# Optimization experiments

Hardware: AMD Instinct MI355X
Metric: run time of the kernel (lower is better)

## Reference

```python
import jax, jax.numpy as jnp
import numpy as np

B, S, F = 64, 1024, 768          # batch, seq = num_patch*patch_size**2, d_model
H, DH = 12, 64                    # heads, head dim = out_dim // d
P2 = 64                           # patch_size ** 2 = attended window length
SCALE = 8.0                       # norm_scale ** 0.5 = (out_dim // d) ** 0.5


def setup_inputs() -> dict:
    key = jax.random.key(0)
    ks = jax.random.split(key, 10)
    std = 0.02
    return {
        "x": jax.random.normal(ks[0], (B, S, F), dtype=jnp.float32),
        # per-head q/k/v projection weights stacked: [H, DH, F] (Linear: y = x @ W.T + b)
        "Wq": jax.random.normal(ks[1], (H, DH, F), dtype=jnp.float32) * std,
        "bq": jax.random.normal(ks[2], (H, DH), dtype=jnp.float32) * std,
        "Wk": jax.random.normal(ks[3], (H, DH, F), dtype=jnp.float32) * std,
        "bk": jax.random.normal(ks[4], (H, DH), dtype=jnp.float32) * std,
        "Wv": jax.random.normal(ks[5], (H, DH, F), dtype=jnp.float32) * std,
        "bv": jax.random.normal(ks[6], (H, DH), dtype=jnp.float32) * std,
        # MHA output projection (only W_MSA[0] is ever used in the stage1 path)
        "Wo": jax.random.normal(ks[7], (F, F), dtype=jnp.float32) * std,
        "bo": jax.random.normal(ks[8], (F,), dtype=jnp.float32) * std,
    }


def reference(x, Wq, bq, Wk, bk, Wv, bv, Wo, bo):
    # stage1 path of SBlock1: only the first window (P2 tokens) goes through
    # MultiHeadAttention (W_MSA[0]); remaining windows are passed through raw
    # and concatenated along the sequence dim.
    xw = x[:, :P2, :]                                    # [B, P2, F]
    q = jnp.einsum('bsf,hdf->bhsd', xw, Wq) + bq[None, :, None, :]
    k = jnp.einsum('bsf,hdf->bhsd', xw, Wk) + bk[None, :, None, :]
    v = jnp.einsum('bsf,hdf->bhsd', xw, Wv) + bv[None, :, None, :]
    scores = jnp.einsum('bhsd,bhtd->bhst', q, k) / SCALE
    attn = jax.nn.softmax(scores, axis=-1)
    o = jnp.einsum('bhst,bhtd->bhsd', attn, v)           # [B, H, P2, DH]
    # heads concatenated along feature dim in order 0..H-1
    o = o.transpose(0, 2, 1, 3).reshape(xw.shape[0], P2, H * DH)
    o = o @ Wo.T + bo                                    # output projection
    return jnp.concatenate([o, x[:, P2:, :]], axis=1)    # [B, S, F]
```

## Files before the change

kernel.cpp:

```cpp
#include <hip/hip_runtime.h>

#define B_   64
#define S_   1024
#define F_   768
#define H_   12
#define DH_  64
#define P2_  64
#define NQKV 2304

using bf16x8 = __attribute__((ext_vector_type(8))) short;
using f32x4  = __attribute__((ext_vector_type(4))) float;

__device__ __forceinline__ unsigned short f2bf(float f) {
    union { float f; unsigned u; } v;
    v.f = f;
    unsigned r = v.u + 0x7FFF + ((v.u >> 16) & 1);
    return (unsigned short)(r >> 16);
}

__device__ __forceinline__ void gll16(const unsigned short* g, unsigned char* l) {
    __builtin_amdgcn_global_load_lds(
        (const __attribute__((address_space(1))) unsigned int*)g,
        (__attribute__((address_space(3))) unsigned int*)l, 16, 0, 0);
}

__device__ __forceinline__ void copy_role(const float* __restrict__ x,
                                          float* __restrict__ out,
                                          int off4, int cnt4, int nblk, int bid) {
    int stride = nblk * 256;
    for (int i = bid * 256 + threadIdx.x; i < cnt4; i += stride) {
        int j = off4 + i;
        int b = j / 184320, r = j - b * 184320;
        int idx = b * 196608 + 12288 + r;
        reinterpret_cast<float4*>(out)[idx] =
            reinterpret_cast<const float4*>(x)[idx];
    }
}

__global__ __launch_bounds__(256) void prep_kernel(
        const float* __restrict__ x,
        const float* __restrict__ Wq, const float* __restrict__ Wk,
        const float* __restrict__ Wv, const float* __restrict__ Wo,
        const float* __restrict__ bq, const float* __restrict__ bk,
        const float* __restrict__ bv,
        unsigned short* __restrict__ xw, unsigned short* __restrict__ Wqkv,
        unsigned short* __restrict__ Wob, float* __restrict__ bqv) {
    const int NW = 786432;
    const int W4 = 147456;
    int i = blockIdx.x * 256 + threadIdx.x;
    if (i < NW) {
        int b = i / 12288, r = i - b * 12288;
        float4 v = reinterpret_cast<const float4*>(x)[b * 196608 + r];
        ushort4 h;
        h.x = f2bf(v.x); h.y = f2bf(v.y); h.z = f2bf(v.z); h.w = f2bf(v.w);
        reinterpret_cast<ushort4*>(xw)[i] = h;
    } else if (i < NW + 3 * W4) {
        int j = i - NW;
        int which = j / W4, local = j - which * W4;
        const float* src = (which == 0) ? Wq : (which == 1) ? Wk : Wv;
        float4 v = reinterpret_cast<const float4*>(src)[local];
        ushort4 h;
        h.x = f2bf(v.x); h.y = f2bf(v.y); h.z = f2bf(v.z); h.w = f2bf(v.w);
        reinterpret_cast<ushort4*>(Wqkv)[j] = h;
    } else if (i < NW + 4 * W4) {
        int local = i - NW - 3 * W4;
        float4 v = reinterpret_cast<const float4*>(Wo)[local];
        ushort4 h;
        h.x = f2bf(v.x); h.y = f2bf(v.y); h.z = f2bf(v.z); h.w = f2bf(v.w);
        reinterpret_cast<ushort4*>(Wob)[local] = h;
    } else if (i < NW + 4 * W4 + 576) {
        int j4 = i - NW - 4 * W4;
        int seg = j4 / 192, local = j4 - seg * 192;
        const float* src = (seg == 0) ? bq : (seg == 1) ? bk : bv;
        reinterpret_cast<float4*>(bqv)[j4] =
            reinterpret_cast<const float4*>(src)[local];
    }
}

template <int BM, int BN, int OUT_MODE>
__device__ __forceinline__ void gemm_body(
        int bx, int by,
        const unsigned short* __restrict__ A, const unsigned short* __restrict__ Bw,
        const float* __restrict__ bias, void* __restrict__ Cout) {
    constexpr int WC = (BN == 128) ? 2 : 1;
    constexpr int WR = 4 / WC;
    constexpr int MI = BM / WR / 16;
    constexpr int NJ = BN / WC / 16;
    constexpr int CA = BM / 32;
    constexpr int CB = BN / 32;
    __shared__ __align__(16) unsigned char lds[(BM + BN) * 128];
    unsigned char* As = lds;
    unsigned char* Bs = lds + BM * 128;
    const int tid  = threadIdx.x;
    const int lane = tid & 63;
    const int w    = tid >> 6;
    const int wr = w / WC, wc = w % WC;
    const int mbase = wr * (BM / WR), nbase = wc * (BN / WC);
    const int m0 = by * BM, n0 = bx * BN;
    const int lr = lane >> 3, lc = lane & 7;

    f32x4 acc[MI][NJ] = {};

    for (int kt = 0; kt < 768; kt += 64) {
        __syncthreads();
#pragma unroll
        for (int p = 0; p < CA; ++p) {
            int row = (w * CA + p) * 8 + lr;
            gll16(A + (size_t)(m0 + row) * 768 + kt + ((lc ^ (row & 7)) << 3),
                  As + (w * CA + p) * 1024);
        }
#pragma unroll
        for (int p = 0; p < CB; ++p) {
            int row = (w * CB + p) * 8 + lr;
            gll16(Bw + (size_t)(n0 + row) * 768 + kt + ((lc ^ (row & 7)) << 3),
                  Bs + (w * CB + p) * 1024);
        }
        __syncthreads();
#pragma unroll
        for (int kk = 0; kk < 2; ++kk) {
            const int g = kk * 4 + (lane >> 4);
            bf16x8 a[MI], b[NJ];
#pragma unroll
            for (int i = 0; i < MI; ++i) {
                int row = mbase + i * 16 + (lane & 15);
                a[i] = *reinterpret_cast<const bf16x8*>(As + row * 128 + ((g ^ (row & 7)) << 4));
            }
#pragma unroll
            for (int j = 0; j < NJ; ++j) {
                int row = nbase + j * 16 + (lane & 15);
                b[j] = *reinterpret_cast<const bf16x8*>(Bs + row * 128 + ((g ^ (row & 7)) << 4));
            }
#pragma unroll
            for (int i = 0; i < MI; ++i)
#pragma unroll
                for (int j = 0; j < NJ; ++j)
                    acc[i][j] = __builtin_amdgcn_mfma_f32_16x16x32_bf16(a[i], b[j], acc[i][j], 0, 0, 0);
        }
    }

    float bj[NJ];
#pragma unroll
    for (int j = 0; j < NJ; ++j) bj[j] = bias[n0 + nbase + j * 16 + (lane & 15)];

#pragma unroll
    for (int i = 0; i < MI; ++i) {
        int mrow = m0 + mbase + i * 16 + ((lane >> 4) << 2);
#pragma unroll
        for (int j = 0; j < NJ; ++j) {
            int n = n0 + nbase + j * 16 + (lane & 15);
#pragma unroll
            for (int r = 0; r < 4; ++r) {
                float v = acc[i][j][r] + bj[j];
                if constexpr (OUT_MODE == 0) {
                    reinterpret_cast<unsigned short*>(Cout)[(size_t)(mrow + r) * 2304 + n] = f2bf(v);
                } else {
                    int m = mrow + r;
                    reinterpret_cast<float*>(Cout)[(size_t)(m >> 6) * 786432 + (m & 63) * 768 + n] = v;
                }
            }
        }
    }
}

__global__ __launch_bounds__(256) void mega_kernel(
        const float* __restrict__ x, float* __restrict__ out,
        const unsigned short* __restrict__ xw, const unsigned short* __restrict__ Wqkv,
        const float* __restrict__ bqv, unsigned short* __restrict__ Y) {
    if (blockIdx.x < 576) {
        gemm_body<128, 128, 0>(blockIdx.x % 18, blockIdx.x / 18, xw, Wqkv, bqv, (void*)Y);
    } else {
        copy_role(x, out, 0, 7077888, 1536, blockIdx.x - 576);
    }
}

__global__ __launch_bounds__(256) void oproj_kernel(
        const unsigned short* __restrict__ Obuf, const unsigned short* __restrict__ Wob,
        const float* __restrict__ bo, float* __restrict__ out,
        const float* __restrict__ x) {
    if (blockIdx.x < 768) {
        gemm_body<64, 64, 1>(blockIdx.x % 12, blockIdx.x / 12, Obuf, Wob, bo, (void*)out);
    } else {
        copy_role(x, out, 8257536, 3538944, 1024, blockIdx.x - 768);
    }
}

__global__ __launch_bounds__(256) void attn_kernel(
        const unsigned short* __restrict__ Y, unsigned short* __restrict__ O,
        const float* __restrict__ x, float* __restrict__ out) {
    if (blockIdx.x >= 768) {
        copy_role(x, out, 7077888, 1179648, 512, blockIdx.x - 768);
        return;
    }
    const int bh = blockIdx.x;
    const int b = bh / 12, h = bh % 12;
    __shared__ __align__(16) unsigned char lds[32768];
    unsigned char* Qs = lds;
    unsigned char* Ks = lds + 8192;
    unsigned char* Vt = lds + 16384;
    unsigned char* Ps = lds + 24576;
    const int tid = threadIdx.x, lane = tid & 63, w = tid >> 6;

    for (int c = tid; c < 512; c += 256) {
        int row = c >> 3, cc = c & 7;
        const unsigned short* src = Y + (size_t)(b * 64 + row) * NQKV + h * 64 + cc * 8;
        *reinterpret_cast<int4*>(Qs + row * 128 + ((cc ^ (row & 7)) << 4)) =
            *reinterpret_cast<const int4*>(src);
        *reinterpret_cast<int4*>(Ks + row * 128 + ((cc ^ (row & 7)) << 4)) =
            *reinterpret_cast<const int4*>(src + 768);
        int4 vv = *reinterpret_cast<const int4*>(src + 1536);
        const unsigned short* vs = reinterpret_cast<const unsigned short*>(&vv);
#pragma unroll
        for (int u = 0; u < 8; ++u) {
            int d = cc * 8 + u;
            *reinterpret_cast<unsigned short*>(
                Vt + d * 128 + (((row >> 3) ^ u) << 4) + ((row & 7) << 1)) = vs[u];
        }
    }
    __syncthreads();

    f32x4 accS[4] = {};
#pragma unroll
    for (int kk = 0; kk < 2; ++kk) {
        const int g = kk * 4 + (lane >> 4);
        int qrow = w * 16 + (lane & 15);
        bf16x8 a = *reinterpret_cast<const bf16x8*>(Qs + qrow * 128 + ((g ^ (qrow & 7)) << 4));
#pragma unroll
        for (int j = 0; j < 4; ++j) {
            int krow = j * 16 + (lane & 15);
            bf16x8 bb = *reinterpret_cast<const bf16x8*>(Ks + krow * 128 + ((g ^ (krow & 7)) << 4));
            accS[j] = __builtin_amdgcn_mfma_f32_16x16x32_bf16(a, bb, accS[j], 0, 0, 0);
        }
    }

#pragma unroll
    for (int r = 0; r < 4; ++r) {
        float v0 = accS[0][r], v1 = accS[1][r], v2 = accS[2][r], v3 = accS[3][r];
        float mx = fmaxf(fmaxf(v0, v1), fmaxf(v2, v3));
        mx = fmaxf(mx, __shfl_xor(mx, 1));
        mx = fmaxf(mx, __shfl_xor(mx, 2));
        mx = fmaxf(mx, __shfl_xor(mx, 4));
        mx = fmaxf(mx, __shfl_xor(mx, 8));
        float p0 = __expf((v0 - mx) * 0.125f);
        float p1 = __expf((v1 - mx) * 0.125f);
        float p2 = __expf((v2 - mx) * 0.125f);
        float p3 = __expf((v3 - mx) * 0.125f);
        float sm = p0 + p1 + p2 + p3;
        sm += __shfl_xor(sm, 1);
        sm += __shfl_xor(sm, 2);
        sm += __shfl_xor(sm, 4);
        sm += __shfl_xor(sm, 8);
        float inv = 1.0f / sm;
        int srow = w * 16 + ((lane >> 4) << 2) + r;
        float pv[4] = {p0 * inv, p1 * inv, p2 * inv, p3 * inv};
#pragma unroll
        for (int j = 0; j < 4; ++j) {
            int t = j * 16 + (lane & 15);
            *reinterpret_cast<unsigned short*>(
                Ps + srow * 128 + (((t >> 3) ^ (srow & 7)) << 4) + ((t & 7) << 1)) = f2bf(pv[j]);
        }
    }
    __syncthreads();

    f32x4 accO[4] = {};
#pragma unroll
    for (int kk = 0; kk < 2; ++kk) {
        const int g = kk * 4 + (lane >> 4);
        int prow = w * 16 + (lane & 15);
        bf16x8 a = *reinterpret_cast<const bf16x8*>(Ps + prow * 128 + ((g ^ (prow & 7)) << 4));
#pragma unroll
        for (int j = 0; j < 4; ++j) {
            int drow = j * 16 + (lane & 15);
            bf16x8 bb = *reinterpret_cast<const bf16x8*>(Vt + drow * 128 + ((g ^ (drow & 7)) << 4));
            accO[j] = __builtin_amdgcn_mfma_f32_16x16x32_bf16(a, bb, accO[j], 0, 0, 0);
        }
    }

#pragma unroll
    for (int j = 0; j < 4; ++j) {
        int d = h * 64 + j * 16 + (lane & 15);
#pragma unroll
        for (int r = 0; r < 4; ++r) {
            int s = w * 16 + ((lane >> 4) << 2) + r;
            O[(size_t)(b * 64 + s) * 768 + d] = f2bf(accO[j][r]);
        }
    }
}

extern "C" void kernel_launch(void* const* d_in, const int* in_sizes, int n_in,
                              void* d_out, int out_size, void* d_ws, size_t ws_size,
                              hipStream_t stream) {
    const float* x  = (const float*)d_in[0];
    const float* Wq = (const float*)d_in[1];
    const float* bq = (const float*)d_in[2];
    const float* Wk = (const float*)d_in[3];
    const float* bk = (const float*)d_in[4];
    const float* Wv = (const float*)d_in[5];
    const float* bv = (const float*)d_in[6];
    const float* Wo = (const float*)d_in[7];
    const float* bo = (const float*)d_in[8];
    float* out = (float*)d_out;
    char* ws = (char*)d_ws;

    unsigned short* xw   = (unsigned short*)(ws);
    unsigned short* Wqkv = (unsigned short*)(ws + 6291456);
    unsigned short* Wob  = (unsigned short*)(ws + 9830400);
    float*          bqv  = (float*)(ws + 11010048);
    unsigned short* Y    = (unsigned short*)(ws + 11019264);
    unsigned short* Obuf = (unsigned short*)(ws + 29893632);

    prep_kernel<<<5379, 256, 0, stream>>>(x, Wq, Wk, Wv, Wo, bq, bk, bv,
                                          xw, Wqkv, Wob, bqv);
    mega_kernel<<<2112, 256, 0, stream>>>(x, out, xw, Wqkv, bqv, Y);
    attn_kernel<<<1280, 256, 0, stream>>>(Y, Obuf, x, out);
    oproj_kernel<<<1792, 256, 0, stream>>>(Obuf, Wob, bo, out, x);
}
```

Baseline: 400.7 us.

## Fuse QKV projection into attention kernel and rebalance passthrough copy

The separate QKV GEMM and attention kernels are merged. Each (batch, head) block now computes its own Q/K/V tile with MFMA straight into LDS, so the bf16 QKV intermediate no longer round-trips through global memory and one launch disappears. The raw passthrough copy of x is redistributed across the prep, fused and output-projection kernels. The cost is that each block rereads the 64-row input window for every head, and there are fewer GEMM blocks with a single-buffered K loop that has two barriers per step.

Result: faster. 388.7 us (-3.0%).

```diff
diff --git a/kernel.cpp b/kernel.cpp
--- a/kernel.cpp
+++ b/kernel.cpp
@@ -6,7 +6,6 @@
 #define H_   12
 #define DH_  64
 #define P2_  64
-#define NQKV 2304
 
 using bf16x8 = __attribute__((ext_vector_type(8))) short;
 using f32x4  = __attribute__((ext_vector_type(4))) float;
@@ -44,9 +43,14 @@
         const float* __restrict__ bq, const float* __restrict__ bk,
         const float* __restrict__ bv,
         unsigned short* __restrict__ xw, unsigned short* __restrict__ Wqkv,
-        unsigned short* __restrict__ Wob, float* __restrict__ bqv) {
+        unsigned short* __restrict__ Wob, float* __restrict__ bqv,
+        float* __restrict__ out) {
     const int NW = 786432;
     const int W4 = 147456;
+    if (blockIdx.x >= 5379) {
+        copy_role(x, out, 0, 2359296, 1024, blockIdx.x - 5379);
+        return;
+    }
     int i = blockIdx.x * 256 + threadIdx.x;
     if (i < NW) {
         int b = i / 12288, r = i - b * 12288;
@@ -77,6 +81,149 @@
     }
 }
 
+__global__ __launch_bounds__(256) void fused_kernel(
+        const unsigned short* __restrict__ xw, const unsigned short* __restrict__ Wqkv,
+        const float* __restrict__ bqv, unsigned short* __restrict__ O,
+        const float* __restrict__ x, float* __restrict__ out) {
+    if (blockIdx.x >= 768) {
+        copy_role(x, out, 2359296, 4718592, 1280, blockIdx.x - 768);
+        return;
+    }
+    const int b = blockIdx.x / 12, h = blockIdx.x % 12;
+    __shared__ __align__(16) unsigned char lds[32768];
+    unsigned char* As = lds;
+    unsigned char* Bs = lds + 8192;
+    unsigned char* Qs = lds;
+    unsigned char* Ks = lds + 8192;
+    unsigned char* Vt = lds + 16384;
+    unsigned char* Ps = lds + 24576;
+    const int tid = threadIdx.x, lane = tid & 63, w = tid >> 6;
+    const int lr = lane >> 3, lc = lane & 7;
+
+    f32x4 acc[12] = {};
+    for (int kt = 0; kt < 768; kt += 64) {
+        __syncthreads();
+#pragma unroll
+        for (int p = 0; p < 2; ++p) {
+            int row = (w * 2 + p) * 8 + lr;
+            gll16(xw + (size_t)(b * 64 + row) * 768 + kt + ((lc ^ (row & 7)) << 3),
+                  As + (w * 2 + p) * 1024);
+        }
+#pragma unroll
+        for (int p = 0; p < 6; ++p) {
+            int idx = w * 6 + p;
+            int row = idx * 8 + lr;
+            int seg = row >> 6, rr = row & 63;
+            gll16(Wqkv + (size_t)(seg * 768 + h * 64 + rr) * 768 + kt + ((lc ^ (row & 7)) << 3),
+                  Bs + idx * 1024);
+        }
+        __syncthreads();
+#pragma unroll
+        for (int kk = 0; kk < 2; ++kk) {
+            const int g = kk * 4 + (lane >> 4);
+            int arow = w * 16 + (lane & 15);
+            bf16x8 a = *reinterpret_cast<const bf16x8*>(As + arow * 128 + ((g ^ (arow & 7)) << 4));
+#pragma unroll
+            for (int j = 0; j < 12; ++j) {
+                int brow = j * 16 + (lane & 15);
+                bf16x8 bb = *reinterpret_cast<const bf16x8*>(Bs + brow * 128 + ((g ^ (brow & 7)) << 4));
+                acc[j] = __builtin_amdgcn_mfma_f32_16x16x32_bf16(a, bb, acc[j], 0, 0, 0);
+            }
+        }
+    }
+
+    __syncthreads();
+#pragma unroll
+    for (int j = 0; j < 12; ++j) {
+        int seg = j >> 2;
+        int d = (j & 3) * 16 + (lane & 15);
+        float bb = bqv[seg * 768 + h * 64 + d];
+#pragma unroll
+        for (int r = 0; r < 4; ++r) {
+            int srow = w * 16 + ((lane >> 4) << 2) + r;
+            unsigned short hv = f2bf(acc[j][r] + bb);
+            if (seg == 0) {
+                *reinterpret_cast<unsigned short*>(Qs + srow * 128 +
+                    (((d >> 3) ^ (srow & 7)) << 4) + ((d & 7) << 1)) = hv;
+            } else if (seg == 1) {
+                *reinterpret_cast<unsigned short*>(Ks + srow * 128 +
+                    (((d >> 3) ^ (srow & 7)) << 4) + ((d & 7) << 1)) = hv;
+            } else {
+                *reinterpret_cast<unsigned short*>(Vt + d * 128 +
+                    (((srow >> 3) ^ (d & 7)) << 4) + ((srow & 7) << 1)) = hv;
+            }
+        }
+    }
+    __syncthreads();
+
+    f32x4 accS[4] = {};
+#pragma unroll
+    for (int kk = 0; kk < 2; ++kk) {
+        const int g = kk * 4 + (lane >> 4);
+        int qrow = w * 16 + (lane & 15);
+        bf16x8 a = *reinterpret_cast<const bf16x8*>(Qs + qrow * 128 + ((g ^ (qrow & 7)) << 4));
+#pragma unroll
+        for (int j = 0; j < 4; ++j) {
+            int krow = j * 16 + (lane & 15);
+            bf16x8 bb = *reinterpret_cast<const bf16x8*>(Ks + krow * 128 + ((g ^ (krow & 7)) << 4));
+            accS[j] = __builtin_amdgcn_mfma_f32_16x16x32_bf16(a, bb, accS[j], 0, 0, 0);
+        }
+    }
+
+#pragma unroll
+    for (int r = 0; r < 4; ++r) {
+        float v0 = accS[0][r], v1 = accS[1][r], v2 = accS[2][r], v3 = accS[3][r];
+        float mx = fmaxf(fmaxf(v0, v1), fmaxf(v2, v3));
+        mx = fmaxf(mx, __shfl_xor(mx, 1));
+        mx = fmaxf(mx, __shfl_xor(mx, 2));
+        mx = fmaxf(mx, __shfl_xor(mx, 4));
+        mx = fmaxf(mx, __shfl_xor(mx, 8));
+        float p0 = __expf((v0 - mx) * 0.125f);
+        float p1 = __expf((v1 - mx) * 0.125f);
+        float p2 = __expf((v2 - mx) * 0.125f);
+        float p3 = __expf((v3 - mx) * 0.125f);
+        float sm = p0 + p1 + p2 + p3;
+        sm += __shfl_xor(sm, 1);
+        sm += __shfl_xor(sm, 2);
+        sm += __shfl_xor(sm, 4);
+        sm += __shfl_xor(sm, 8);
+        float inv = 1.0f / sm;
+        int srow = w * 16 + ((lane >> 4) << 2) + r;
+        float pv[4] = {p0 * inv, p1 * inv, p2 * inv, p3 * inv};
+#pragma unroll
+        for (int j = 0; j < 4; ++j) {
+            int t = j * 16 + (lane & 15);
+            *reinterpret_cast<unsigned short*>(
+                Ps + srow * 128 + (((t >> 3) ^ (srow & 7)) << 4) + ((t & 7) << 1)) = f2bf(pv[j]);
+        }
+    }
+    __syncthreads();
+
+    f32x4 accO[4] = {};
+#pragma unroll
+    for (int kk = 0; kk < 2; ++kk) {
+        const int g = kk * 4 + (lane >> 4);
+        int prow = w * 16 + (lane & 15);
+        bf16x8 a = *reinterpret_cast<const bf16x8*>(Ps + prow * 128 + ((g ^ (prow & 7)) << 4));
+#pragma unroll
+        for (int j = 0; j < 4; ++j) {
+            int drow = j * 16 + (lane & 15);
+            bf16x8 bb = *reinterpret_cast<const bf16x8*>(Vt + drow * 128 + ((g ^ (drow & 7)) << 4));
+            accO[j] = __builtin_amdgcn_mfma_f32_16x16x32_bf16(a, bb, accO[j], 0, 0, 0);
+        }
+    }
+
+#pragma unroll
+    for (int j = 0; j < 4; ++j) {
+        int d = h * 64 + j * 16 + (lane & 15);
+#pragma unroll
+        for (int r = 0; r < 4; ++r) {
+            int s = w * 16 + ((lane >> 4) << 2) + r;
+            O[(size_t)(b * 64 + s) * 768 + d] = f2bf(accO[j][r]);
+        }
+    }
+}
+
 template <int BM, int BN, int OUT_MODE>
 __device__ __forceinline__ void gemm_body(
         int bx, int by,
@@ -152,24 +299,13 @@
             for (int r = 0; r < 4; ++r) {
                 float v = acc[i][j][r] + bj[j];
                 if constexpr (OUT_MODE == 0) {
-                    reinterpret_cast<unsigned short*>(Cout)[(size_t)(mrow + r) * 2304 + n] = f2bf(v);
+                    reinterpret_cast<unsigned short*>(Cout)[(size_t)(mrow + r) * 768 + n] = f2bf(v);
                 } else {
                     int m = mrow + r;
                     reinterpret_cast<float*>(Cout)[(size_t)(m >> 6) * 786432 + (m & 63) * 768 + n] = v;
                 }
             }
         }
-    }
-}
-
-__global__ __launch_bounds__(256) void mega_kernel(
-        const float* __restrict__ x, float* __restrict__ out,
-        const unsigned short* __restrict__ xw, const unsigned short* __restrict__ Wqkv,
-        const float* __restrict__ bqv, unsigned short* __restrict__ Y) {
-    if (blockIdx.x < 576) {
-        gemm_body<128, 128, 0>(blockIdx.x % 18, blockIdx.x / 18, xw, Wqkv, bqv, (void*)Y);
-    } else {
-        copy_role(x, out, 0, 7077888, 1536, blockIdx.x - 576);
     }
 }
 
@@ -180,109 +316,7 @@
     if (blockIdx.x < 768) {
         gemm_body<64, 64, 1>(blockIdx.x % 12, blockIdx.x / 12, Obuf, Wob, bo, (void*)out);
     } else {
-        copy_role(x, out, 8257536, 3538944, 1024, blockIdx.x - 768);
-    }
-}
-
-__global__ __launch_bounds__(256) void attn_kernel(
-        const unsigned short* __restrict__ Y, unsigned short* __restrict__ O,
-        const float* __restrict__ x, float* __restrict__ out) {
-    if (blockIdx.x >= 768) {
-        copy_role(x, out, 7077888, 1179648, 512, blockIdx.x - 768);
-        return;
-    }
-    const int bh = blockIdx.x;
-    const int b = bh / 12, h = bh % 12;
-    __shared__ __align__(16) unsigned char lds[32768];
-    unsigned char* Qs = lds;
-    unsigned char* Ks = lds + 8192;
-    unsigned char* Vt = lds + 16384;
-    unsigned char* Ps = lds + 24576;
-    const int tid = threadIdx.x, lane = tid & 63, w = tid >> 6;
-
-    for (int c = tid; c < 512; c += 256) {
-        int row = c >> 3, cc = c & 7;
-        const unsigned short* src = Y + (size_t)(b * 64 + row) * NQKV + h * 64 + cc * 8;
-        *reinterpret_cast<int4*>(Qs + row * 128 + ((cc ^ (row & 7)) << 4)) =
-            *reinterpret_cast<const int4*>(src);
-        *reinterpret_cast<int4*>(Ks + row * 128 + ((cc ^ (row & 7)) << 4)) =
-            *reinterpret_cast<const int4*>(src + 768);
-        int4 vv = *reinterpret_cast<const int4*>(src + 1536);
-        const unsigned short* vs = reinterpret_cast<const unsigned short*>(&vv);
-#pragma unroll
-        for (int u = 0; u < 8; ++u) {
-            int d = cc * 8 + u;
-            *reinterpret_cast<unsigned short*>(
-                Vt + d * 128 + (((row >> 3) ^ u) << 4) + ((row & 7) << 1)) = vs[u];
-        }
-    }
-    __syncthreads();
-
-    f32x4 accS[4] = {};
-#pragma unroll
-    for (int kk = 0; kk < 2; ++kk) {
-        const int g = kk * 4 + (lane >> 4);
-        int qrow = w * 16 + (lane & 15);
-        bf16x8 a = *reinterpret_cast<const bf16x8*>(Qs + qrow * 128 + ((g ^ (qrow & 7)) << 4));
-#pragma unroll
-        for (int j = 0; j < 4; ++j) {
-            int krow = j * 16 + (lane & 15);
-            bf16x8 bb = *reinterpret_cast<const bf16x8*>(Ks + krow * 128 + ((g ^ (krow & 7)) << 4));
-            accS[j] = __builtin_amdgcn_mfma_f32_16x16x32_bf16(a, bb, accS[j], 0, 0, 0);
-        }
-    }
-
-#pragma unroll
-    for (int r = 0; r < 4; ++r) {
-        float v0 = accS[0][r], v1 = accS[1][r], v2 = accS[2][r], v3 = accS[3][r];
-        float mx = fmaxf(fmaxf(v0, v1), fmaxf(v2, v3));
-        mx = fmaxf(mx, __shfl_xor(mx, 1));
-        mx = fmaxf(mx, __shfl_xor(mx, 2));
-        mx = fmaxf(mx, __shfl_xor(mx, 4));
-        mx = fmaxf(mx, __shfl_xor(mx, 8));
-        float p0 = __expf((v0 - mx) * 0.125f);
-        float p1 = __expf((v1 - mx) * 0.125f);
-        float p2 = __expf((v2 - mx) * 0.125f);
-        float p3 = __expf((v3 - mx) * 0.125f);
-        float sm = p0 + p1 + p2 + p3;
-        sm += __shfl_xor(sm, 1);
-        sm += __shfl_xor(sm, 2);
-        sm += __shfl_xor(sm, 4);
-        sm += __shfl_xor(sm, 8);
-        float inv = 1.0f / sm;
-        int srow = w * 16 + ((lane >> 4) << 2) + r;
-        float pv[4] = {p0 * inv, p1 * inv, p2 * inv, p3 * inv};
-#pragma unroll
-        for (int j = 0; j < 4; ++j) {
-            int t = j * 16 + (lane & 15);
-            *reinterpret_cast<unsigned short*>(
-                Ps + srow * 128 + (((t >> 3) ^ (srow & 7)) << 4) + ((t & 7) << 1)) = f2bf(pv[j]);
-        }
-    }
-    __syncthreads();
-
-    f32x4 accO[4] = {};
-#pragma unroll
-    for (int kk = 0; kk < 2; ++kk) {
-        const int g = kk * 4 + (lane >> 4);
-        int prow = w * 16 + (lane & 15);
-        bf16x8 a = *reinterpret_cast<const bf16x8*>(Ps + prow * 128 + ((g ^ (prow & 7)) << 4));
-#pragma unroll
-        for (int j = 0; j < 4; ++j) {
-            int drow = j * 16 + (lane & 15);
-            bf16x8 bb = *reinterpret_cast<const bf16x8*>(Vt + drow * 128 + ((g ^ (drow & 7)) << 4));
-            accO[j] = __builtin_amdgcn_mfma_f32_16x16x32_bf16(a, bb, accO[j], 0, 0, 0);
-        }
-    }
-
-#pragma unroll
-    for (int j = 0; j < 4; ++j) {
-        int d = h * 64 + j * 16 + (lane & 15);
-#pragma unroll
-        for (int r = 0; r < 4; ++r) {
-            int s = w * 16 + ((lane >> 4) << 2) + r;
-            O[(size_t)(b * 64 + s) * 768 + d] = f2bf(accO[j][r]);
-        }
+        copy_role(x, out, 7077888, 4718592, 1280, blockIdx.x - 768);
     }
 }
 
@@ -305,12 +339,10 @@
     unsigned short* Wqkv = (unsigned short*)(ws + 6291456);
     unsigned short* Wob  = (unsigned short*)(ws + 9830400);
     float*          bqv  = (float*)(ws + 11010048);
-    unsigned short* Y    = (unsigned short*)(ws + 11019264);
-    unsigned short* Obuf = (unsigned short*)(ws + 29893632);
-
-    prep_kernel<<<5379, 256, 0, stream>>>(x, Wq, Wk, Wv, Wo, bq, bk, bv,
-                                          xw, Wqkv, Wob, bqv);
-    mega_kernel<<<2112, 256, 0, stream>>>(x, out, xw, Wqkv, bqv, Y);
-    attn_kernel<<<1280, 256, 0, stream>>>(Y, Obuf, x, out);
-    oproj_kernel<<<1792, 256, 0, stream>>>(Obuf, Wob, bo, out, x);
-}
+    unsigned short* Obuf = (unsigned short*)(ws + 11019264);
+
+    prep_kernel<<<6403, 256, 0, stream>>>(x, Wq, Wk, Wv, Wo, bq, bk, bv,
+                                          xw, Wqkv, Wob, bqv, out);
+    fused_kernel<<<2048, 256, 0, stream>>>(xw, Wqkv, bqv, Obuf, x, out);
+    oproj_kernel<<<2048, 256, 0, stream>>>(Obuf, Wob, bo, out, x);
+}
```
